# Kernel tuning notes

Hardware: AMD Instinct MI355X
Metric: run time of the kernel (lower is better)

Reference implementation:

```python
import jax, jax.numpy as jnp
import numpy as np

N, E, G = 5000, 10000, 200
EPS = 1e-5


def _nnconv(x, edge_attr, src, dst, w1, b1, w2, b2, root, bias, din, dout):
    # edge MLP -> per-edge weight matrix [E, din, dout]
    h = jax.nn.relu(edge_attr @ w1 + b1)
    We = (h @ w2 + b2).reshape(-1, din, dout)
    # gather source node feats, per-edge bmm, scatter-mean to targets
    msg = jnp.einsum('ei,eio->eo', x[src], We)  # [E, dout]
    s = jax.ops.segment_sum(msg, dst, num_segments=N)
    cnt = jax.ops.segment_sum(jnp.ones((msg.shape[0],), msg.dtype), dst, num_segments=N)
    agg = s / jnp.maximum(cnt, 1.0)[:, None]
    return agg + x @ root + bias


def _bn(x, g, b, m, v):
    return (x - m) * (g / jnp.sqrt(v + EPS)) + b


def setup_inputs() -> dict:
    key = jax.random.key(0)
    ks = iter(jax.random.split(key, 64))
    d = {}
    d['x'] = jax.random.normal(next(ks), (N, 15), jnp.float32)
    d['edge_attr'] = jax.random.normal(next(ks), (E, 3), jnp.float32)
    d['edge_index'] = jax.random.randint(next(ks), (2, E), 0, N, jnp.int32)
    d['batch'] = jnp.sort(jax.random.randint(next(ks), (N,), 0, G, jnp.int32))
    d['atom_num'] = jnp.zeros((G,), jnp.int32)
    dims = [(15, 64), (64, 128), (128, 256)]
    for l, (din, dout) in enumerate(dims, start=1):
        d[f'nn{l}_w1'] = jax.random.normal(next(ks), (3, 32), jnp.float32) * 0.1
        d[f'nn{l}_b1'] = jnp.zeros((32,), jnp.float32)
        d[f'nn{l}_w2'] = jax.random.normal(next(ks), (32, din * dout), jnp.float32) * 0.05
        d[f'nn{l}_b2'] = jnp.zeros((din * dout,), jnp.float32)
        d[f'root{l}'] = jax.random.normal(next(ks), (din, dout), jnp.float32) * 0.1
        d[f'bias{l}'] = jnp.zeros((dout,), jnp.float32)
        d[f'bn{l}_g'] = jnp.ones((dout,), jnp.float32)
        d[f'bn{l}_b'] = jnp.zeros((dout,), jnp.float32)
        d[f'bn{l}_m'] = jnp.zeros((dout,), jnp.float32)
        d[f'bn{l}_v'] = jnp.ones((dout,), jnp.float32)
    d['mlp_w'] = jax.random.normal(next(ks), (256, 200), jnp.float32) * 0.05
    d['mlp_b'] = jnp.zeros((200,), jnp.float32)
    return d


def reference(x, edge_attr, edge_index, batch, atom_num,
              nn1_w1, nn1_b1, nn1_w2, nn1_b2, root1, bias1, bn1_g, bn1_b, bn1_m, bn1_v,
              nn2_w1, nn2_b1, nn2_w2, nn2_b2, root2, bias2, bn2_g, bn2_b, bn2_m, bn2_v,
              nn3_w1, nn3_b1, nn3_w2, nn3_b2, root3, bias3, bn3_g, bn3_b, bn3_m, bn3_v,
              mlp_w, mlp_b):
    src, dst = edge_index[0], edge_index[1]
    h = _nnconv(x, edge_attr, src, dst, nn1_w1, nn1_b1, nn1_w2, nn1_b2, root1, bias1, 15, 64)
    h = jax.nn.relu(_bn(h, bn1_g, bn1_b, bn1_m, bn1_v))
    h = _nnconv(h, edge_attr, src, dst, nn2_w1, nn2_b1, nn2_w2, nn2_b2, root2, bias2, 64, 128)
    h = jax.nn.relu(_bn(h, bn2_g, bn2_b, bn2_m, bn2_v))
    h = _nnconv(h, edge_attr, src, dst, nn3_w1, nn3_b1, nn3_w2, nn3_b2, root3, bias3, 128, 256)
    h = jax.nn.relu(_bn(h, bn3_g, bn3_b, bn3_m, bn3_v))
    node_rep = h
    # per-graph node counts, exclusive cumulative offsets
    ones = jnp.ones((N,), h.dtype)
    counts = jax.ops.segment_sum(ones, batch, num_segments=G)  # [G]
    offsets = (jnp.cumsum(counts) - counts).astype(jnp.int32)
    idx = atom_num + offsets
    node_embedding = node_rep[idx]  # [G, 256]
    # global mean pool
    gsum = jax.ops.segment_sum(h, batch, num_segments=G)
    graph_embedding = gsum / jnp.maximum(counts, 1.0)[:, None]
    h_new = 0.5 * graph_embedding + node_embedding
    out = h_new @ mlp_w + mlp_b
    return out, node_embedding
```

## Files before the change

kernel.cpp:

```cpp
#include <hip/hip_runtime.h>
#include <stdint.h>

#define DEVINL __device__ __forceinline__

typedef __attribute__((ext_vector_type(8))) __bf16 bf16x8;
typedef __attribute__((ext_vector_type(8))) short s16x8;
typedef __attribute__((ext_vector_type(4))) float f32x4;

constexpr int NN = 5000;
constexpr int NE = 10000;
constexpr int NG = 200;
constexpr int BM = 64;
constexpr int MBLK = (NE + BM - 1) / BM;
constexpr int EROWS = MBLK * BM;
constexpr int SBLK = (NN + BM - 1) / BM;
constexpr int SROWS = SBLK * BM;
constexpr int NKP = 36;
constexpr int PHKT = 4;

DEVINL short f2bf(float f) {
  union { float f; unsigned u; } v; v.f = f;
  unsigned u = v.u + 0x7fffu + ((v.u >> 16) & 1u);
  return (short)(u >> 16);
}

DEVINL void gload16(const void* g, void* l) {
  __builtin_amdgcn_global_load_lds(
      (const __attribute__((address_space(1))) void*)g,
      (__attribute__((address_space(3))) void*)l, 16, 0, 0);
}


__global__ void prep(const int* dst, const int* batch, const float* x0,
                     float* cnt, float* gcnt, short* xbf0) {
  int idx = blockIdx.x * 256 + threadIdx.x;
  if (idx < NE) atomicAdd(&cnt[dst[idx]], 1.0f);
  if (idx < NN) atomicAdd(&gcnt[batch[idx]], 1.0f);
  if (idx < NN * 32) {
    int n = idx >> 5, i = idx & 31;
    xbf0[idx] = (i < 15) ? f2bf(x0[n * 15 + i]) : (short)0;
  }
}

__global__ void node_scan(const float* cnt, int* noff, int* fill) {
  __shared__ int s[1024];
  __shared__ int carry;
  int t = threadIdx.x;
  if (t == 0) carry = 0;
  __syncthreads();
  for (int c0 = 0; c0 < NN; c0 += 1024) {
    int i = c0 + t;
    int v = (i < NN) ? (int)cnt[i] : 0;
    s[t] = v;
    __syncthreads();
    for (int d = 1; d < 1024; d <<= 1) {
      int u = (t >= d) ? s[t - d] : 0;
      __syncthreads();
      s[t] += u;
      __syncthreads();
    }
    if (i < NN) { noff[i] = carry + s[t] - v; fill[i] = 0; }
    __syncthreads();
    if (t == 0) carry += s[1023];
    __syncthreads();
  }
}

__global__ void csr_fill(const int* dst, const int* noff, int* fill, int* elist) {
  int e = blockIdx.x * 256 + threadIdx.x;
  if (e < NE) {
    int n = dst[e];
    int p = noff[n] + atomicAdd(&fill[n], 1);
    elist[p] = e;
  }
}


__global__ void edge_mlp_all(const float* ea,
                             const float* w1a, const float* b1a,
                             const float* w1b, const float* b1b,
                             const float* w1c, const float* b1c,
                             short* hta, short* htb, short* htc) {
  int L = blockIdx.z;
  const float* w1 = (L == 0) ? w1a : (L == 1) ? w1b : w1c;
  const float* b1 = (L == 0) ? b1a : (L == 1) ? b1b : b1c;
  short* ht = (L == 0) ? hta : (L == 1) ? htb : htc;
  __shared__ float w1s[3];
  __shared__ float b1s;
  int t = threadIdx.x;
  int k = blockIdx.y;
  if (t < 3 && k < 32) w1s[t] = w1[t * 32 + k];
  if (t == 0 && k < 32) b1s = b1[k];
  __syncthreads();
  int e = blockIdx.x * 256 + t;
  if (e >= EROWS) return;
  float v = 0.f;
  if (e < NE) {
    if (k < 32) {
      float a = b1s + ea[e * 3] * w1s[0] + ea[e * 3 + 1] * w1s[1] +
                ea[e * 3 + 2] * w1s[2];
      v = a > 0.f ? a : 0.f;
    } else if (k == 32) {
      v = 1.0f;
    }
  }
  ht[(size_t)k * EROWS + e] = f2bf(v);
}


template <int DIN_DATA, int DIN_PAD, int DOUT>
DEVINL void buildB_one(int idx, const float* w2, const float* b2,
                       const float* root, short* Bp) {
  int cc = idx & 3;
  int n = (idx >> 2) % DOUT;
  int kt = (idx >> 2) / DOUT;
  int kap0 = kt * 32 + cc * 8;
  s16x8 v;
#pragma unroll
  for (int j = 0; j < 8; ++j) {
    int kap = kap0 + j;
    int k = kap / DIN_PAD, i = kap % DIN_PAD;
    float val = 0.f;
    if (i < DIN_DATA && k <= 33)
      val = (k < 32) ? w2[(size_t)(k * DIN_DATA + i) * DOUT + n]
                     : (k == 32) ? b2[(size_t)i * DOUT + n]
                                 : root[(size_t)i * DOUT + n];
    v[j] = f2bf(val);
  }
  int swz = cc ^ ((n >> 1) & 3);
  *(s16x8*)((char*)Bp + (size_t)kt * DOUT * 64 + n * 64 + swz * 16) = v;
}

constexpr int BCH1 = (NKP * 32 / 8) * 64;
constexpr int BCH2 = (NKP * 64 / 8) * 128;
constexpr int BCH3 = (NKP * 128 / 8) * 256;

__global__ void build_B_all(const float* w2a, const float* b2a, const float* ra,
                            const float* w2b, const float* b2b, const float* rb,
                            const float* w2c, const float* b2c, const float* rc,
                            short* Bp1, short* Bp2, short* Bp3) {
  int idx = blockIdx.x * 256 + threadIdx.x;
  if (idx < BCH1) {
    buildB_one<15, 32, 64>(idx, w2a, b2a, ra, Bp1);
  } else if (idx < BCH1 + BCH2) {
    buildB_one<64, 64, 128>(idx - BCH1, w2b, b2b, rb, Bp2);
  } else if (idx < BCH1 + BCH2 + BCH3) {
    buildB_one<128, 128, 256>(idx - BCH1 - BCH2, w2c, b2c, rc, Bp3);
  }
}


template <int DIN_PAD, int DOUT, int NSPLIT, int NKPE>
__launch_bounds__(512)
__global__ void fused_gemm(const short* xbf, const short* ht, const short* Bp,
                           const int* srcI, float* Pout) {
  constexpr int NI = DIN_PAD / 32;
  constexpr int ROWB = DIN_PAD * 2;
  constexpr int CHPR = ROWB / 16;
  constexpr int CHLOG = (CHPR == 4) ? 2 : (CHPR == 8) ? 3 : 4;
  constexpr int SWZM = (CHPR >= 8) ? 7 : 3;
  constexpr int DOUT_L = DOUT / NSPLIT;
  constexpr int MT = 2;
  constexpr int KT_TOTAL = NKPE * NI;
  constexpr int NPH = KT_TOTAL / PHKT;
  static_assert(KT_TOTAL % PHKT == 0, "phase align");
  static_assert(PHKT % NI == 0 || NI % PHKT == 0, "k align");
  constexpr int PHB = PHKT * DOUT_L * 64;
  constexpr int CPK = DOUT_L * 4;
  constexpr int CH = PHKT * CPK;
  constexpr int XGB = BM * ROWB;
  constexpr int SMB = (XGB > 2 * PHB) ? XGB : 2 * PHB;

  __shared__ __align__(16) char smem[SMB];
  __shared__ __align__(16) short hs[NKPE * BM];
  __shared__ int src_s[BM];

  const int t = threadIdx.x, lane = t & 63, w = t >> 6;
  const int wm = w >> 2, wn = w & 3;
  const bool isSelf = (blockIdx.x >= MBLK);
  const int m0 = (isSelf ? (blockIdx.x - MBLK) : blockIdx.x) * BM;
  const int bn0 = blockIdx.y * DOUT_L;
  if (t < BM) {
    int r = m0 + t;
    src_s[t] = isSelf ? ((r < NN) ? r : 0) : ((r < NE) ? srcI[r] : 0);
  }
  __syncthreads();

  constexpr int XCH = BM * CHPR;
#pragma unroll
  for (int rd = 0; rd < (XCH + 511) / 512; ++rd) {
    int L = rd * 512 + t;
    if (XCH % 512 == 0 || L < XCH) {
      int r = L >> CHLOG, pch = L & (CHPR - 1);
      int j = pch ^ (r & SWZM);
      gload16((const char*)xbf + (size_t)src_s[r] * ROWB + j * 16,
              (char*)smem + (size_t)L * 16);
    }
  }
  if (!isSelf && t < NKPE * (BM / 8)) {
    int kl = t >> 3, c = t & 7;
    gload16((const char*)ht + ((size_t)kl * EROWS + m0) * 2 + c * 16,
            (char*)hs + (size_t)t * 16);
  }
  __syncthreads();

  bf16x8 afr[NI][MT];
#pragma unroll
  for (int ii = 0; ii < NI; ++ii)
#pragma unroll
    for (int mt = 0; mt < MT; ++mt) {
      int r = wm * 32 + mt * 16 + (lane & 15);
      int c = ii * 4 + (lane >> 4);
      int pos = c ^ (r & SWZM);
      afr[ii][mt] = *(const bf16x8*)((const char*)smem + r * ROWB + pos * 16);
    }
  asm volatile("s_waitcnt lgkmcnt(0)" ::: "memory");
  __builtin_amdgcn_sched_barrier(0);
  __builtin_amdgcn_s_barrier();

  const char* Bg = (const char*)Bp + (size_t)bn0 * 64;

  f32x4 msg[MT], part[MT];
#pragma unroll
  for (int mt = 0; mt < MT; ++mt)
#pragma unroll
    for (int i = 0; i < 4; ++i) { msg[mt][i] = 0.f; part[mt][i] = 0.f; }

  if (isSelf) {
    constexpr int KT0 = 33 * NI;
    constexpr int CHS = NI * CPK;
#pragma unroll
    for (int cc = 0; cc < (CHS + 511) / 512; ++cc) {
      int idx = cc * 512 + t;
      if (CHS % 512 == 0 || idx < CHS) {
        int ktl = idx / CPK, win = idx % CPK;
        gload16(Bg + (size_t)(KT0 + ktl) * (DOUT * 64) + (size_t)win * 16,
                (char*)smem + (size_t)idx * 16);
      }
    }
    asm volatile("s_waitcnt vmcnt(0)" ::: "memory");
    __builtin_amdgcn_s_barrier();
    __builtin_amdgcn_sched_barrier(0);
#pragma unroll
    for (int j = 0; j < NI; ++j) {
      bf16x8 bfr;
      {
        int n = wn * 16 + (lane & 15);
        int cch = (lane >> 4) ^ ((n >> 1) & 3);
        bfr = *(const bf16x8*)((const char*)smem + j * (DOUT_L * 64) + n * 64 +
                               cch * 16);
      }
#pragma unroll
      for (int mt = 0; mt < MT; ++mt)
        msg[mt] = __builtin_amdgcn_mfma_f32_16x16x32_bf16(afr[j][mt], bfr,
                                                          msg[mt], 0, 0, 0);
    }
    float* P = Pout + (size_t)(EROWS + m0) * DOUT + bn0;
#pragma unroll
    for (int mt = 0; mt < MT; ++mt) {
      int col = wn * 16 + (lane & 15);
#pragma unroll
      for (int reg = 0; reg < 4; ++reg) {
        int r = wm * 32 + mt * 16 + (lane >> 4) * 4 + reg;
        P[(size_t)r * DOUT + col] = msg[mt][reg];
      }
    }
    return;
  }

  auto stageB = [&](int ph, int buf) {
    char* dstB = (char*)smem + buf * PHB;
#pragma unroll
    for (int cc = 0; cc < CH / 512; ++cc) {
      int idx = cc * 512 + t;
      int ktl = idx / CPK;
      int win = idx % CPK;
      gload16(Bg + (size_t)(ph * PHKT + ktl) * (DOUT * 64) + (size_t)win * 16,
              dstB + (size_t)idx * 16);
    }
  };

  stageB(0, 0);
  int cur = 0;
  for (int ph = 0; ph < NPH; ++ph) {
    if (ph + 1 < NPH) {
      stageB(ph + 1, cur ^ 1);
      asm volatile("s_waitcnt vmcnt(2)" ::: "memory");
    } else {
      asm volatile("s_waitcnt vmcnt(0)" ::: "memory");
    }
    __builtin_amdgcn_s_barrier();
    __builtin_amdgcn_sched_barrier(0);
#pragma unroll
    for (int j = 0; j < PHKT; ++j) {
      const int kt = ph * PHKT + j;
      bf16x8 bfr;
      {
        int n = wn * 16 + (lane & 15);
        int cch = (lane >> 4) ^ ((n >> 1) & 3);
        bfr = *(const bf16x8*)((const char*)smem + cur * PHB +
                               j * (DOUT_L * 64) + n * 64 + cch * 16);
      }
#pragma unroll
      for (int mt = 0; mt < MT; ++mt)
        part[mt] = __builtin_amdgcn_mfma_f32_16x16x32_bf16(
            afr[j % NI][mt], bfr, part[mt], 0, 0, 0);
      if ((j % NI) == NI - 1) {
        int kl = kt / NI;
#pragma unroll
        for (int mt = 0; mt < MT; ++mt) {
          int rb = wm * 32 + mt * 16 + (lane >> 4) * 4;
          ushort4 hv = *(const ushort4*)((const char*)hs + (size_t)(kl * BM + rb) * 2);
          float h0, h1, h2, h3;
          { union { unsigned u; float f; } c;
            c.u = (unsigned)hv.x << 16; h0 = c.f;
            c.u = (unsigned)hv.y << 16; h1 = c.f;
            c.u = (unsigned)hv.z << 16; h2 = c.f;
            c.u = (unsigned)hv.w << 16; h3 = c.f; }
          msg[mt][0] += h0 * part[mt][0];
          msg[mt][1] += h1 * part[mt][1];
          msg[mt][2] += h2 * part[mt][2];
          msg[mt][3] += h3 * part[mt][3];
#pragma unroll
          for (int i = 0; i < 4; ++i) part[mt][i] = 0.f;
        }
      }
    }
    __builtin_amdgcn_sched_barrier(0);
    __builtin_amdgcn_s_barrier();
    cur ^= 1;
  }
  float* P = Pout + (size_t)m0 * DOUT + bn0;
#pragma unroll
  for (int mt = 0; mt < MT; ++mt) {
    int col = wn * 16 + (lane & 15);
#pragma unroll
    for (int reg = 0; reg < 4; ++reg) {
      int r = wm * 32 + mt * 16 + (lane >> 4) * 4 + reg;
      P[(size_t)r * DOUT + col] = msg[mt][reg];
    }
  }
}


template <int DOUT>
__launch_bounds__(256)
__global__ void post_node(const float* P, const float* cnt, const int* noff,
                          const int* elist, const float* bias, const float* bg,
                          const float* bb, const float* bm, const float* bv,
                          float* xout, short* xbf) {
  constexpr int NPB = 8;
  constexpr int OS = 256 / DOUT;
  constexpr int NPT = NPB / OS;
  __shared__ int offs[NPB], cnts[NPB];
  int n0 = blockIdx.x * NPB;
  int t = threadIdx.x;
  int o = t % DOUT;
  int ng = t / DOUT;
  if (t < NPB) {
    int n = n0 + t;
    offs[t] = (n < NN) ? noff[n] : 0;
    cnts[t] = (n < NN) ? (int)cnt[n] : 0;
  }
  __syncthreads();
  float bi = bias[o];
  float scale = bg[o] * rsqrtf(bv[o] + 1e-5f);
  float mo = bm[o], bo = bb[o];
#pragma unroll
  for (int q = 0; q < NPT; ++q) {
    int nn = ng + q * OS;
    int n = n0 + nn;
    if (n >= NN) continue;
    int off = offs[nn], c = cnts[nn];
    float s = 0.f;
    for (int j = 0; j < c; ++j) {
      int e = elist[off + j];
      s += P[(size_t)e * DOUT + o];
    }
    float selfv = P[(size_t)(EROWS + n) * DOUT + o];
    float accv = s / fmaxf((float)c, 1.f) + selfv + bi;
    float v = (accv - mo) * scale + bo;
    v = v > 0.f ? v : 0.f;
    if (xout) xout[(size_t)n * DOUT + o] = v;
    if (xbf) xbf[(size_t)n * DOUT + o] = f2bf(v);
  }
}


__global__ void finish(const float* gcnt, const int* atom, const float* x3,
                       const float* mw, const float* mb, float* out) {
  __shared__ float red[256];
  __shared__ float hnew[256];
  int g = blockIdx.x, t = threadIdx.x;
  red[t] = (t < NG && t < g) ? gcnt[t] : 0.f;
  __syncthreads();
#pragma unroll
  for (int d = 128; d > 0; d >>= 1) {
    if (t < d) red[t] += red[t + d];
    __syncthreads();
  }
  int st = (int)red[0];
  int cn = (int)gcnt[g];
  int id = st + atom[g];
  id = id < 0 ? 0 : (id > NN - 1 ? NN - 1 : id);
  float s = 0.f;
  for (int n = st; n < st + cn; ++n) s += x3[(size_t)n * 256 + t];
  float ge = s / fmaxf((float)cn, 1.f);
  float ne = x3[(size_t)id * 256 + t];
  out[40000 + g * 256 + t] = ne;
  hnew[t] = 0.5f * ge + ne;
  __syncthreads();
  if (t < 200) {
    float a = mb[t];
#pragma unroll 8
    for (int oo = 0; oo < 256; ++oo) a += hnew[oo] * mw[(size_t)oo * 200 + t];
    out[g * 200 + t] = a;
  }
}


template <int DIN_PAD, int DOUT, int NSPLIT, int NKPE>
static void run_layer(void* const* d_in, int l, const int* srcI,
                      const short* xbf_in, float* xout_f32, short* xbf_out,
                      float* Pbuf, const float* cnt, const int* noff,
                      const int* elist, const short* ht, const short* Bp,
                      hipStream_t stream) {
  int base = 5 + (l - 1) * 10;
  const float* bias = (const float*)d_in[base + 5];
  const float* bg = (const float*)d_in[base + 6];
  const float* bb = (const float*)d_in[base + 7];
  const float* bm = (const float*)d_in[base + 8];
  const float* bv = (const float*)d_in[base + 9];

  fused_gemm<DIN_PAD, DOUT, NSPLIT, NKPE>
      <<<dim3(MBLK + SBLK, NSPLIT), 512, 0, stream>>>(xbf_in, ht, Bp, srcI, Pbuf);
  post_node<DOUT><<<(NN + 7) / 8, 256, 0, stream>>>(
      Pbuf, cnt, noff, elist, bias, bg, bb, bm, bv, xout_f32, xbf_out);
}

extern "C" void kernel_launch(void* const* d_in, const int* in_sizes, int n_in,
                              void* d_out, int out_size, void* d_ws, size_t ws_size,
                              hipStream_t stream) {
  (void)in_sizes; (void)n_in; (void)out_size; (void)ws_size;
  const float* x0 = (const float*)d_in[0];
  const float* ea = (const float*)d_in[1];
  const int* eidx = (const int*)d_in[2];
  const int* batch = (const int*)d_in[3];
  const int* atom = (const int*)d_in[4];
  const float* mw = (const float*)d_in[35];
  const float* mb = (const float*)d_in[36];
  const int* srcI = eidx;
  const int* dstI = eidx + NE;
  float* out = (float*)d_out;

  char* p = (char*)d_ws;
  auto alloc = [&](size_t bytes) {
    char* r = p;
    p += (bytes + 255) & ~size_t(255);
    return r;
  };
  float* xA = (float*)alloc((size_t)NN * 256 * 4);
  float* Pbuf = (float*)alloc((size_t)(EROWS + SROWS) * 256 * 4);
  float* cnt = (float*)alloc(NN * 4);
  int* noff = (int*)alloc(NN * 4);
  int* fill = (int*)alloc(NN * 4);
  int* elist = (int*)alloc(NE * 4);
  float* gcnt = (float*)alloc(NG * 4);
  short* ht1 = (short*)alloc((size_t)NKP * EROWS * 2);
  short* ht2 = (short*)alloc((size_t)NKP * EROWS * 2);
  short* ht3 = (short*)alloc((size_t)NKP * EROWS * 2);
  short* Bp1 = (short*)alloc((size_t)NKP * 32 * 64 * 2);
  short* Bp2 = (short*)alloc((size_t)NKP * 64 * 128 * 2);
  short* Bp3 = (short*)alloc((size_t)NKP * 128 * 256 * 2);
  short* xbf0 = (short*)alloc((size_t)NN * 32 * 2);
  short* xbfA = (short*)alloc((size_t)NN * 64 * 2);
  short* xbfB = (short*)alloc((size_t)NN * 128 * 2);

  hipMemsetAsync(cnt, 0, NN * 4, stream);
  hipMemsetAsync(gcnt, 0, NG * 4, stream);
  prep<<<(NN * 32 + 255) / 256, 256, 0, stream>>>(dstI, batch, x0, cnt, gcnt, xbf0);
  node_scan<<<1, 1024, 0, stream>>>(cnt, noff, fill);
  csr_fill<<<(NE + 255) / 256, 256, 0, stream>>>(dstI, noff, fill, elist);
  edge_mlp_all<<<dim3((EROWS + 255) / 256, NKP, 3), 256, 0, stream>>>(
      ea, (const float*)d_in[5], (const float*)d_in[6],
      (const float*)d_in[15], (const float*)d_in[16],
      (const float*)d_in[25], (const float*)d_in[26], ht1, ht2, ht3);
  build_B_all<<<(BCH1 + BCH2 + BCH3 + 255) / 256, 256, 0, stream>>>(
      (const float*)d_in[7], (const float*)d_in[8], (const float*)d_in[9],
      (const float*)d_in[17], (const float*)d_in[18], (const float*)d_in[19],
      (const float*)d_in[27], (const float*)d_in[28], (const float*)d_in[29],
      Bp1, Bp2, Bp3);

  run_layer<32, 64, 1, 36>(d_in, 1, srcI, xbf0, (float*)nullptr, xbfA, Pbuf,
                           cnt, noff, elist, ht1, Bp1, stream);
  run_layer<64, 128, 2, 34>(d_in, 2, srcI, xbfA, (float*)nullptr, xbfB, Pbuf,
                            cnt, noff, elist, ht2, Bp2, stream);
  run_layer<128, 256, 4, 33>(d_in, 3, srcI, xbfB, xA, (short*)nullptr, Pbuf,
                             cnt, noff, elist, ht3, Bp3, stream);

  finish<<<NG, 256, 0, stream>>>(gcnt, atom, xA, mw, mb, out);
}
```

Before: 271.5 us.

## Merge setup kernels, single-pass node scan, triple-buffer B staging in GEMM

Folds the prep, edge MLP and B-packing kernels into one setup launch, with the edge MLP now looping over all 36 k columns per thread instead of one block per column. The node scan becomes one pass in which each thread sums a contiguous chunk serially, replacing the five chunked scan passes. The fused GEMM moves from double to triple buffering of B phases in LDS and issues loads two phases ahead with adjusted vmcnt waits. The goals are fewer launches and better hiding of global load latency, at the cost of more LDS per block, which may lower occupancy.

```diff
diff --git a/kernel.cpp b/kernel.cpp
--- a/kernel.cpp
+++ b/kernel.cpp
@@ -17,6 +17,7 @@
 constexpr int SROWS = SBLK * BM;
 constexpr int NKP = 36;
 constexpr int PHKT = 4;
+constexpr int NBUF = 3;
 
 DEVINL short f2bf(float f) {
   union { float f; unsigned u; } v; v.f = f;
@@ -28,83 +29,6 @@
   __builtin_amdgcn_global_load_lds(
       (const __attribute__((address_space(1))) void*)g,
       (__attribute__((address_space(3))) void*)l, 16, 0, 0);
-}
-
-
-__global__ void prep(const int* dst, const int* batch, const float* x0,
-                     float* cnt, float* gcnt, short* xbf0) {
-  int idx = blockIdx.x * 256 + threadIdx.x;
-  if (idx < NE) atomicAdd(&cnt[dst[idx]], 1.0f);
-  if (idx < NN) atomicAdd(&gcnt[batch[idx]], 1.0f);
-  if (idx < NN * 32) {
-    int n = idx >> 5, i = idx & 31;
-    xbf0[idx] = (i < 15) ? f2bf(x0[n * 15 + i]) : (short)0;
-  }
-}
-
-__global__ void node_scan(const float* cnt, int* noff, int* fill) {
-  __shared__ int s[1024];
-  __shared__ int carry;
-  int t = threadIdx.x;
-  if (t == 0) carry = 0;
-  __syncthreads();
-  for (int c0 = 0; c0 < NN; c0 += 1024) {
-    int i = c0 + t;
-    int v = (i < NN) ? (int)cnt[i] : 0;
-    s[t] = v;
-    __syncthreads();
-    for (int d = 1; d < 1024; d <<= 1) {
-      int u = (t >= d) ? s[t - d] : 0;
-      __syncthreads();
-      s[t] += u;
-      __syncthreads();
-    }
-    if (i < NN) { noff[i] = carry + s[t] - v; fill[i] = 0; }
-    __syncthreads();
-    if (t == 0) carry += s[1023];
-    __syncthreads();
-  }
-}
-
-__global__ void csr_fill(const int* dst, const int* noff, int* fill, int* elist) {
-  int e = blockIdx.x * 256 + threadIdx.x;
-  if (e < NE) {
-    int n = dst[e];
-    int p = noff[n] + atomicAdd(&fill[n], 1);
-    elist[p] = e;
-  }
-}
-
-
-__global__ void edge_mlp_all(const float* ea,
-                             const float* w1a, const float* b1a,
-                             const float* w1b, const float* b1b,
-                             const float* w1c, const float* b1c,
-                             short* hta, short* htb, short* htc) {
-  int L = blockIdx.z;
-  const float* w1 = (L == 0) ? w1a : (L == 1) ? w1b : w1c;
-  const float* b1 = (L == 0) ? b1a : (L == 1) ? b1b : b1c;
-  short* ht = (L == 0) ? hta : (L == 1) ? htb : htc;
-  __shared__ float w1s[3];
-  __shared__ float b1s;
-  int t = threadIdx.x;
-  int k = blockIdx.y;
-  if (t < 3 && k < 32) w1s[t] = w1[t * 32 + k];
-  if (t == 0 && k < 32) b1s = b1[k];
-  __syncthreads();
-  int e = blockIdx.x * 256 + t;
-  if (e >= EROWS) return;
-  float v = 0.f;
-  if (e < NE) {
-    if (k < 32) {
-      float a = b1s + ea[e * 3] * w1s[0] + ea[e * 3 + 1] * w1s[1] +
-                ea[e * 3 + 2] * w1s[2];
-      v = a > 0.f ? a : 0.f;
-    } else if (k == 32) {
-      v = 1.0f;
-    }
-  }
-  ht[(size_t)k * EROWS + e] = f2bf(v);
 }
 
 
@@ -134,18 +58,100 @@
 constexpr int BCH1 = (NKP * 32 / 8) * 64;
 constexpr int BCH2 = (NKP * 64 / 8) * 128;
 constexpr int BCH3 = (NKP * 128 / 8) * 256;
-
-__global__ void build_B_all(const float* w2a, const float* b2a, const float* ra,
-                            const float* w2b, const float* b2b, const float* rb,
-                            const float* w2c, const float* b2c, const float* rc,
-                            short* Bp1, short* Bp2, short* Bp3) {
-  int idx = blockIdx.x * 256 + threadIdx.x;
-  if (idx < BCH1) {
-    buildB_one<15, 32, 64>(idx, w2a, b2a, ra, Bp1);
-  } else if (idx < BCH1 + BCH2) {
-    buildB_one<64, 64, 128>(idx - BCH1, w2b, b2b, rb, Bp2);
-  } else if (idx < BCH1 + BCH2 + BCH3) {
-    buildB_one<128, 128, 256>(idx - BCH1 - BCH2, w2c, b2c, rc, Bp3);
+constexpr int EMB = (EROWS + 255) / 256;
+constexpr int PREPB = (NN * 32 + 255) / 256;
+constexpr int BLDB = (BCH1 + BCH2 + BCH3 + 255) / 256;
+
+
+__global__ void setup(const float* ea, const int* dst, const int* batch,
+                      const float* x0,
+                      const float* w1a, const float* b1a,
+                      const float* w1b, const float* b1b,
+                      const float* w1c, const float* b1c,
+                      const float* w2a, const float* b2a, const float* ra,
+                      const float* w2b, const float* b2b, const float* rb,
+                      const float* w2c, const float* b2c, const float* rc,
+                      short* hta, short* htb, short* htc,
+                      short* Bp1, short* Bp2, short* Bp3,
+                      float* cnt, float* gcnt, short* xbf0) {
+  int b = blockIdx.x, t = threadIdx.x;
+  if (b < 3 * EMB) {
+    int L = b / EMB, eb = b % EMB;
+    const float* w1 = (L == 0) ? w1a : (L == 1) ? w1b : w1c;
+    const float* b1 = (L == 0) ? b1a : (L == 1) ? b1b : b1c;
+    short* ht = (L == 0) ? hta : (L == 1) ? htb : htc;
+    int e = eb * 256 + t;
+    if (e >= EROWS) return;
+    bool ve = e < NE;
+    float a0 = 0, a1 = 0, a2 = 0;
+    if (ve) { a0 = ea[e * 3]; a1 = ea[e * 3 + 1]; a2 = ea[e * 3 + 2]; }
+    for (int k = 0; k < NKP; ++k) {
+      float v = 0.f;
+      if (ve) {
+        if (k < 32) {
+          float x = b1[k] + a0 * w1[k] + a1 * w1[32 + k] + a2 * w1[64 + k];
+          v = x > 0.f ? x : 0.f;
+        } else if (k == 32) {
+          v = 1.0f;
+        }
+      }
+      ht[(size_t)k * EROWS + e] = f2bf(v);
+    }
+  } else if (b < 3 * EMB + PREPB) {
+    int idx = (b - 3 * EMB) * 256 + t;
+    if (idx < NE) atomicAdd(&cnt[dst[idx]], 1.0f);
+    if (idx < NN) atomicAdd(&gcnt[batch[idx]], 1.0f);
+    if (idx < NN * 32) {
+      int n = idx >> 5, i = idx & 31;
+      xbf0[idx] = (i < 15) ? f2bf(x0[n * 15 + i]) : (short)0;
+    }
+  } else {
+    int idx = (b - 3 * EMB - PREPB) * 256 + t;
+    if (idx < BCH1) {
+      buildB_one<15, 32, 64>(idx, w2a, b2a, ra, Bp1);
+    } else if (idx < BCH1 + BCH2) {
+      buildB_one<64, 64, 128>(idx - BCH1, w2b, b2b, rb, Bp2);
+    } else if (idx < BCH1 + BCH2 + BCH3) {
+      buildB_one<128, 128, 256>(idx - BCH1 - BCH2, w2c, b2c, rc, Bp3);
+    }
+  }
+}
+
+
+__global__ void node_scan(const float* cnt, int* noff, int* fill) {
+  constexpr int PT = (NN + 1023) / 1024;
+  __shared__ int s[1024];
+  int t = threadIdx.x;
+  int loc[PT];
+  int sum = 0;
+#pragma unroll
+  for (int q = 0; q < PT; ++q) {
+    int i = t * PT + q;
+    loc[q] = sum;
+    sum += (i < NN) ? (int)cnt[i] : 0;
+  }
+  s[t] = sum;
+  __syncthreads();
+  for (int d = 1; d < 1024; d <<= 1) {
+    int u = (t >= d) ? s[t - d] : 0;
+    __syncthreads();
+    s[t] += u;
+    __syncthreads();
+  }
+  int base = s[t] - sum;
+#pragma unroll
+  for (int q = 0; q < PT; ++q) {
+    int i = t * PT + q;
+    if (i < NN) { noff[i] = base + loc[q]; fill[i] = 0; }
+  }
+}
+
+__global__ void csr_fill(const int* dst, const int* noff, int* fill, int* elist) {
+  int e = blockIdx.x * 256 + threadIdx.x;
+  if (e < NE) {
+    int n = dst[e];
+    int p = noff[n] + atomicAdd(&fill[n], 1);
+    elist[p] = e;
   }
 }
 
@@ -169,7 +175,7 @@
   constexpr int CPK = DOUT_L * 4;
   constexpr int CH = PHKT * CPK;
   constexpr int XGB = BM * ROWB;
-  constexpr int SMB = (XGB > 2 * PHB) ? XGB : 2 * PHB;
+  constexpr int SMB = (XGB > NBUF * PHB) ? XGB : NBUF * PHB;
 
   __shared__ __align__(16) char smem[SMB];
   __shared__ __align__(16) short hs[NKPE * BM];
@@ -281,16 +287,19 @@
   };
 
   stageB(0, 0);
-  int cur = 0;
+  if (NPH > 1) stageB(1, 1);
+  if (NPH > 2) stageB(2, 2);
   for (int ph = 0; ph < NPH; ++ph) {
-    if (ph + 1 < NPH) {
-      stageB(ph + 1, cur ^ 1);
+    if (ph + 2 < NPH) {
+      asm volatile("s_waitcnt vmcnt(4)" ::: "memory");
+    } else if (ph + 1 < NPH) {
       asm volatile("s_waitcnt vmcnt(2)" ::: "memory");
     } else {
       asm volatile("s_waitcnt vmcnt(0)" ::: "memory");
     }
     __builtin_amdgcn_s_barrier();
     __builtin_amdgcn_sched_barrier(0);
+    const char* buf = (const char*)smem + (ph % NBUF) * PHB;
 #pragma unroll
     for (int j = 0; j < PHKT; ++j) {
       const int kt = ph * PHKT + j;
@@ -298,8 +307,7 @@
       {
         int n = wn * 16 + (lane & 15);
         int cch = (lane >> 4) ^ ((n >> 1) & 3);
-        bfr = *(const bf16x8*)((const char*)smem + cur * PHB +
-                               j * (DOUT_L * 64) + n * 64 + cch * 16);
+        bfr = *(const bf16x8*)(buf + j * (DOUT_L * 64) + n * 64 + cch * 16);
       }
 #pragma unroll
       for (int mt = 0; mt < MT; ++mt)
@@ -328,7 +336,7 @@
     }
     __builtin_amdgcn_sched_barrier(0);
     __builtin_amdgcn_s_barrier();
-    cur ^= 1;
+    if (ph + NBUF < NPH) stageB(ph + NBUF, (ph + NBUF) % NBUF);
   }
   float* P = Pout + (size_t)m0 * DOUT + bn0;
 #pragma unroll
@@ -478,18 +486,17 @@
 
   hipMemsetAsync(cnt, 0, NN * 4, stream);
   hipMemsetAsync(gcnt, 0, NG * 4, stream);
-  prep<<<(NN * 32 + 255) / 256, 256, 0, stream>>>(dstI, batch, x0, cnt, gcnt, xbf0);
-  node_scan<<<1, 1024, 0, stream>>>(cnt, noff, fill);
-  csr_fill<<<(NE + 255) / 256, 256, 0, stream>>>(dstI, noff, fill, elist);
-  edge_mlp_all<<<dim3((EROWS + 255) / 256, NKP, 3), 256, 0, stream>>>(
-      ea, (const float*)d_in[5], (const float*)d_in[6],
+  setup<<<3 * EMB + PREPB + BLDB, 256, 0, stream>>>(
+      ea, dstI, batch, x0,
+      (const float*)d_in[5], (const float*)d_in[6],
       (const float*)d_in[15], (const float*)d_in[16],
-      (const float*)d_in[25], (const float*)d_in[26], ht1, ht2, ht3);
-  build_B_all<<<(BCH1 + BCH2 + BCH3 + 255) / 256, 256, 0, stream>>>(
+      (const float*)d_in[25], (const float*)d_in[26],
       (const float*)d_in[7], (const float*)d_in[8], (const float*)d_in[9],
       (const float*)d_in[17], (const float*)d_in[18], (const float*)d_in[19],
       (const float*)d_in[27], (const float*)d_in[28], (const float*)d_in[29],
-      Bp1, Bp2, Bp3);
+      ht1, ht2, ht3, Bp1, Bp2, Bp3, cnt, gcnt, xbf0);
+  node_scan<<<1, 1024, 0, stream>>>(cnt, noff, fill);
+  csr_fill<<<(NE + 255) / 256, 256, 0, stream>>>(dstI, noff, fill, elist);
 
   run_layer<32, 64, 1, 36>(d_in, 1, srcI, xbf0, (float*)nullptr, xbfA, Pbuf,
                            cnt, noff, elist, ht1, Bp1, stream);
```

New measurement: 260.9 us. 1.04x faster.
